# Kernel tuning notes

Hardware: AMD Instinct MI355X
Metric: run time of the kernel (lower is better)

Reference implementation:

```python
import jax, jax.numpy as jnp
import numpy as np

SIGMA = 1.0


def setup_inputs() -> dict:
    key = jax.random.key(0)
    k1, k2 = jax.random.split(key)
    B, N = 32, 1024
    logits = jax.random.normal(k1, (B, N, 1), dtype=jnp.float32)
    labels = jax.random.randint(k2, (B, N, 1), 0, 5).astype(jnp.float32)
    item_mask = jnp.ones((B, N), dtype=bool)
    return {"logits": logits, "labels": labels, "item_mask": item_mask}


def _ndcg_weights(y, sorted_indices):
    # y: (B, N) relevance labels; sorted_indices: (B, N) argsort of scores desc
    b, n = y.shape
    gains = 2.0 ** y - 1.0                                   # (B, N)
    ideal_sorted = -jnp.sort(-gains, axis=-1)                # descending sort
    positions = jnp.arange(1, n + 1, dtype=y.dtype)          # (N,)
    discounts = 1.0 / jnp.log2(positions + 1.0)              # (N,)  (k=None)
    idcg = jnp.clip((ideal_sorted * discounts).sum(-1, keepdims=True), 1e-8)
    # scatter: ranks[b, sorted_indices[b, j]] = j + 1
    ranks = jnp.zeros_like(y).at[jnp.arange(b)[:, None], sorted_indices].set(
        jnp.broadcast_to(positions, (b, n)))
    disc_i = 1.0 / jnp.log2(ranks + 1.0)                     # (B, N)
    gain_diff = jnp.abs(gains[:, :, None] - gains[:, None, :])   # (B, N, N)
    disc_diff = jnp.abs(disc_i[:, :, None] - disc_i[:, None, :]) # (B, N, N)
    return gain_diff * disc_diff / idcg[..., None]


def reference(logits, labels, item_mask):
    scores = logits[..., 0]                                  # (B, N)
    y = labels[..., 0].astype(jnp.float32)                   # (B, N)
    n = scores.shape[1]
    sorted_indices = jnp.argsort(-jax.lax.stop_gradient(scores), axis=-1)
    s_ij = SIGMA * (scores[:, :, None] - scores[:, None, :])     # (B, N, N)
    y_ij = jnp.sign(y[:, :, None] - y[:, None, :])               # (B, N, N)
    weights = _ndcg_weights(y, sorted_indices)                   # (B, N, N)
    pair_loss = jax.nn.softplus(-y_ij * s_ij) * weights          # log1p(exp(.))
    triu = jnp.triu(jnp.ones((n, n), dtype=bool), k=1)
    valid = item_mask[:, :, None] & item_mask[:, None, :]
    pair_loss = pair_loss * triu[None] * valid
    loss = pair_loss.sum(axis=(1, 2))                            # (B,)
    return loss.mean()                                           # reduction='mean'
```

## Files before the change

kernel.cpp:

```cpp
#include <hip/hip_runtime.h>
#include <math.h>


#define N    1024
#define T    1024
#define BPB  8

typedef unsigned int u32;

__device__ __forceinline__ float pair_term(const float4 fi, const float4 fj)
{
    const float ds  = fi.x - fj.x;
    const float dg  = fi.y - fj.y;
    const float arg = (dg > 0.0f) ? -ds : ds;
    const float sp  = __logf(1.0f + __expf(arg));
    return sp * fabsf(dg) * fabsf(fi.z - fj.z);
}

__device__ __forceinline__ u32 flipkey(float s)
{
    const u32 u = __float_as_uint(s);
    const u32 m = (u >> 31) ? ~u : (u | 0x80000000u);
    return ~m;
}

__global__ __launch_bounds__(T) void lrank_fused(const float* __restrict__ logits,
                                                 const float* __restrict__ labels,
                                                 float* __restrict__ out,
                                                 float inv_B)
{
    __shared__ float4 it[N];
    __shared__ u32    shi[N];
    __shared__ u32    slo[N];
    __shared__ float  wred[16];
    __shared__ float  wredI[16];
    __shared__ int    hist[5];
    __shared__ float  sidcg;

    const int b  = blockIdx.y;
    const int c  = blockIdx.x;
    const int t  = threadIdx.x;
    const int wv = t >> 6;
    const int ln = t & 63;

    if (t < 5) hist[t] = 0;
    __syncthreads();

    if (t < 256) {
        const float4 sv = ((const float4*)(logits + b * N))[t];
        const float4 yv = ((const float4*)(labels + b * N))[t];
        it[4*t+0] = make_float4(sv.x, exp2f(yv.x) - 1.0f, 0.0f, 0.0f);
        it[4*t+1] = make_float4(sv.y, exp2f(yv.y) - 1.0f, 0.0f, 0.0f);
        it[4*t+2] = make_float4(sv.z, exp2f(yv.z) - 1.0f, 0.0f, 0.0f);
        it[4*t+3] = make_float4(sv.w, exp2f(yv.w) - 1.0f, 0.0f, 0.0f);
        shi[4*t+0] = flipkey(sv.x);  slo[4*t+0] = 4*t+0;
        shi[4*t+1] = flipkey(sv.y);  slo[4*t+1] = 4*t+1;
        shi[4*t+2] = flipkey(sv.z);  slo[4*t+2] = 4*t+2;
        shi[4*t+3] = flipkey(sv.w);  slo[4*t+3] = 4*t+3;
    } else if (t < 512) {
        const int uu = t - 256;
        const float4 yv = ((const float4*)(labels + b * N))[uu];
        atomicAdd(&hist[(int)yv.x], 1);
        atomicAdd(&hist[(int)yv.y], 1);
        atomicAdd(&hist[(int)yv.z], 1);
        atomicAdd(&hist[(int)yv.w], 1);
    }
    __syncthreads();

    {
        const int c4 = hist[4];
        const int c3 = c4 + hist[3];
        const int c2 = c3 + hist[2];
        const int c1 = c2 + hist[1];
        const float gain = (t < c4) ? 15.0f : (t < c3) ? 7.0f
                         : (t < c2) ? 3.0f  : (t < c1) ? 1.0f : 0.0f;
        float ip = gain / __log2f((float)(t + 2));
        #pragma unroll
        for (int off = 32; off; off >>= 1) ip += __shfl_xor(ip, off);
        if (ln == 0) wredI[wv] = ip;
    }

    for (int k = 2; k <= N; k <<= 1) {
        for (int jj = k >> 1; jj > 0; jj >>= 1) {
            if (t < 512) {
                const int i  = ((t & ~(jj - 1)) << 1) | (t & (jj - 1));
                const int ix = i | jj;
                const u32 ha = shi[i],  hb = shi[ix];
                const u32 la = slo[i],  lb = slo[ix];
                const bool up  = ((i & k) == 0);
                const bool agt = (ha > hb) || (ha == hb && la > lb);
                if (agt == up) {
                    shi[i] = hb; shi[ix] = ha;
                    slo[i] = lb; slo[ix] = la;
                }
            }
            __syncthreads();
        }
    }

    it[slo[t]].z = 1.0f / __log2f((float)(t + 2));
    __syncthreads();
    if (t == 0) {
        float s = 0.0f;
        #pragma unroll
        for (int i2 = 0; i2 < 16; ++i2) s += wredI[i2];
        sidcg = fmaxf(s, 1e-8f);
    }
    __syncthreads();

    const int rA = c * 64 + 4 * wv;
    const int rB = 1023 - rA;
    const float4 fr0 = it[rA],     fr1 = it[rA + 1];
    const float4 fr2 = it[rA + 2], fr3 = it[rA + 3];
    const float4 gr0 = it[rB],     gr1 = it[rB - 1];
    const float4 gr2 = it[rB - 2], gr3 = it[rB - 3];

    float acc = 0.0f;
    for (int j = rA + 1 + ln; j < N; j += 64) {
        const float4 fj = it[j];
        acc += pair_term(fr0, fj);
        if (j > rA + 1) acc += pair_term(fr1, fj);
        if (j > rA + 2) acc += pair_term(fr2, fj);
        if (j > rA + 3) acc += pair_term(fr3, fj);
    }
    for (int j = rB - 2 + ln; j < N; j += 64) {
        const float4 fj = it[j];
        acc += pair_term(gr3, fj);
        if (j > rB - 2) acc += pair_term(gr2, fj);
        if (j > rB - 1) acc += pair_term(gr1, fj);
        if (j > rB)     acc += pair_term(gr0, fj);
    }

    #pragma unroll
    for (int off = 32; off; off >>= 1) acc += __shfl_xor(acc, off);
    if (ln == 0) wred[wv] = acc;
    __syncthreads();
    if (t == 0) {
        float s = 0.0f;
        #pragma unroll
        for (int i2 = 0; i2 < 16; ++i2) s += wred[i2];
        atomicAdd(out, s * inv_B / sidcg);
    }
}

extern "C" void kernel_launch(void* const* d_in, const int* in_sizes, int n_in,
                              void* d_out, int out_size, void* d_ws, size_t ws_size,
                              hipStream_t stream) {
    const float* logits = (const float*)d_in[0];
    const float* labels = (const float*)d_in[1];
    const int B = in_sizes[0] / N;
    float* out = (float*)d_out;

    hipMemsetAsync(out, 0, sizeof(float), stream);
    lrank_fused<<<dim3(BPB, B), dim3(T), 0, stream>>>(logits, labels, out,
                                                      1.0f / (float)B);
}
```

Baseline: 85.40 us.

## Register-resident bitonic sort with wave shuffles, ballot histogram, base-2 softplus

Replaces the shared-memory bitonic sort, which had a barrier per step and only 512 active threads, with a per-thread 64-bit key sort. Stages with stride under 64 use wave shuffles and larger strides exchange through LDS, which cuts the number of block-wide barriers. The label histogram now uses ballot/popcount instead of per-element LDS atomics. Scores are prescaled by log2(e) so softplus can use exp2/log2, with ln2 folded into the final scale. The triangular diagonal pairs are peeled into a small prologue so the main pair loops run without branches. In exchange, the kernel adds shuffle traffic and more complex index logic.

After: 79.88 us. -6.5%, faster.

```diff
diff --git a/kernel.cpp b/kernel.cpp
--- a/kernel.cpp
+++ b/kernel.cpp
@@ -7,15 +7,7 @@
 #define BPB  8
 
 typedef unsigned int u32;
-
-__device__ __forceinline__ float pair_term(const float4 fi, const float4 fj)
-{
-    const float ds  = fi.x - fj.x;
-    const float dg  = fi.y - fj.y;
-    const float arg = (dg > 0.0f) ? -ds : ds;
-    const float sp  = __logf(1.0f + __expf(arg));
-    return sp * fabsf(dg) * fabsf(fi.z - fj.z);
-}
+typedef unsigned long long u64;
 
 __device__ __forceinline__ u32 flipkey(float s)
 {
@@ -24,14 +16,29 @@
     return ~m;
 }
 
+__device__ __forceinline__ u64 shfl_xor_u64(u64 v, int m)
+{
+    const int lo = __shfl_xor((int)(u32)v, m);
+    const int hi = __shfl_xor((int)(u32)(v >> 32), m);
+    return ((u64)(u32)hi << 32) | (u32)lo;
+}
+
+__device__ __forceinline__ float pair_term(const float4 fi, const float4 fj)
+{
+    const float d1  = fj.x - fi.x;
+    const float dg  = fi.y - fj.y;
+    const float arg = (dg > 0.0f) ? d1 : -d1;
+    const float sp2 = log2f(1.0f + exp2f(arg));
+    return sp2 * fabsf(dg) * fabsf(fi.z - fj.z);
+}
+
 __global__ __launch_bounds__(T) void lrank_fused(const float* __restrict__ logits,
                                                  const float* __restrict__ labels,
                                                  float* __restrict__ out,
-                                                 float inv_B)
+                                                 float scale)
 {
     __shared__ float4 it[N];
-    __shared__ u32    shi[N];
-    __shared__ u32    slo[N];
+    __shared__ u64    sk[N];
     __shared__ float  wred[16];
     __shared__ float  wredI[16];
     __shared__ int    hist[5];
@@ -46,24 +53,16 @@
     if (t < 5) hist[t] = 0;
     __syncthreads();
 
-    if (t < 256) {
-        const float4 sv = ((const float4*)(logits + b * N))[t];
-        const float4 yv = ((const float4*)(labels + b * N))[t];
-        it[4*t+0] = make_float4(sv.x, exp2f(yv.x) - 1.0f, 0.0f, 0.0f);
-        it[4*t+1] = make_float4(sv.y, exp2f(yv.y) - 1.0f, 0.0f, 0.0f);
-        it[4*t+2] = make_float4(sv.z, exp2f(yv.z) - 1.0f, 0.0f, 0.0f);
-        it[4*t+3] = make_float4(sv.w, exp2f(yv.w) - 1.0f, 0.0f, 0.0f);
-        shi[4*t+0] = flipkey(sv.x);  slo[4*t+0] = 4*t+0;
-        shi[4*t+1] = flipkey(sv.y);  slo[4*t+1] = 4*t+1;
-        shi[4*t+2] = flipkey(sv.z);  slo[4*t+2] = 4*t+2;
-        shi[4*t+3] = flipkey(sv.w);  slo[4*t+3] = 4*t+3;
-    } else if (t < 512) {
-        const int uu = t - 256;
-        const float4 yv = ((const float4*)(labels + b * N))[uu];
-        atomicAdd(&hist[(int)yv.x], 1);
-        atomicAdd(&hist[(int)yv.y], 1);
-        atomicAdd(&hist[(int)yv.z], 1);
-        atomicAdd(&hist[(int)yv.w], 1);
+    const float s = logits[b * N + t];
+    const float y = labels[b * N + t];
+    it[t] = make_float4(s * 1.4426950408889634f, exp2f(y) - 1.0f, 0.0f, 0.0f);
+    u64 K = ((u64)flipkey(s) << 32) | (u32)t;
+
+    const int yi = (int)y;
+    #pragma unroll
+    for (int v = 0; v < 5; ++v) {
+        const u64 m = __ballot(yi == v);
+        if (ln == 0) atomicAdd(&hist[v], (int)__popcll(m));
     }
     __syncthreads();
 
@@ -80,31 +79,43 @@
         if (ln == 0) wredI[wv] = ip;
     }
 
-    for (int k = 2; k <= N; k <<= 1) {
-        for (int jj = k >> 1; jj > 0; jj >>= 1) {
-            if (t < 512) {
-                const int i  = ((t & ~(jj - 1)) << 1) | (t & (jj - 1));
-                const int ix = i | jj;
-                const u32 ha = shi[i],  hb = shi[ix];
-                const u32 la = slo[i],  lb = slo[ix];
-                const bool up  = ((i & k) == 0);
-                const bool agt = (ha > hb) || (ha == hb && la > lb);
-                if (agt == up) {
-                    shi[i] = hb; shi[ix] = ha;
-                    slo[i] = lb; slo[ix] = la;
-                }
-            }
+    #pragma unroll
+    for (int k = 2; k <= 64; k <<= 1) {
+        #pragma unroll
+        for (int jj = k >> 1; jj; jj >>= 1) {
+            const u64 PK = shfl_xor_u64(K, jj);
+            const bool keepmin = (((t & k) == 0) == ((t & jj) == 0));
+            const bool mine_gt = (K > PK);
+            if (mine_gt == keepmin) K = PK;
+        }
+    }
+    #pragma unroll
+    for (int k = 128; k <= 1024; k <<= 1) {
+        #pragma unroll
+        for (int jj = k >> 1; jj >= 64; jj >>= 1) {
+            sk[t] = K;
             __syncthreads();
+            const u64 PK = sk[t ^ jj];
+            const bool keepmin = (((t & k) == 0) == ((t & jj) == 0));
+            const bool mine_gt = (K > PK);
+            if (mine_gt == keepmin) K = PK;
+            __syncthreads();
+        }
+        #pragma unroll
+        for (int jj = 32; jj; jj >>= 1) {
+            const u64 PK = shfl_xor_u64(K, jj);
+            const bool keepmin = (((t & k) == 0) == ((t & jj) == 0));
+            const bool mine_gt = (K > PK);
+            if (mine_gt == keepmin) K = PK;
         }
     }
 
-    it[slo[t]].z = 1.0f / __log2f((float)(t + 2));
-    __syncthreads();
+    it[(int)(K & 1023u)].z = 1.0f / __log2f((float)(t + 2));
     if (t == 0) {
-        float s = 0.0f;
+        float si = 0.0f;
         #pragma unroll
-        for (int i2 = 0; i2 < 16; ++i2) s += wredI[i2];
-        sidcg = fmaxf(s, 1e-8f);
+        for (int i = 0; i < 16; ++i) si += wredI[i];
+        sidcg = fmaxf(si, 1e-8f);
     }
     __syncthreads();
 
@@ -116,19 +127,30 @@
     const float4 gr2 = it[rB - 2], gr3 = it[rB - 3];
 
     float acc = 0.0f;
-    for (int j = rA + 1 + ln; j < N; j += 64) {
+
+    if (ln < 12) {
+        const int p = (ln >= 6) ? ln - 6 : ln;
+        const int a = (p < 3) ? 0 : (p < 5) ? 1 : 2;
+        const int bb = (p == 0) ? 1 : (p == 1) ? 2 : (p == 2) ? 3
+                     : (p == 3) ? 2 : 3;
+        const int i1 = (ln < 6) ? rA + a  : rB - a;
+        const int i2 = (ln < 6) ? rA + bb : rB - bb;
+        acc += pair_term(it[i1], it[i2]);
+    }
+
+    for (int j = rA + 4 + ln; j < N; j += 64) {
         const float4 fj = it[j];
         acc += pair_term(fr0, fj);
-        if (j > rA + 1) acc += pair_term(fr1, fj);
-        if (j > rA + 2) acc += pair_term(fr2, fj);
-        if (j > rA + 3) acc += pair_term(fr3, fj);
+        acc += pair_term(fr1, fj);
+        acc += pair_term(fr2, fj);
+        acc += pair_term(fr3, fj);
     }
-    for (int j = rB - 2 + ln; j < N; j += 64) {
+    for (int j = rB + 1 + ln; j < N; j += 64) {
         const float4 fj = it[j];
+        acc += pair_term(gr0, fj);
+        acc += pair_term(gr1, fj);
+        acc += pair_term(gr2, fj);
         acc += pair_term(gr3, fj);
-        if (j > rB - 2) acc += pair_term(gr2, fj);
-        if (j > rB - 1) acc += pair_term(gr1, fj);
-        if (j > rB)     acc += pair_term(gr0, fj);
     }
 
     #pragma unroll
@@ -136,10 +158,10 @@
     if (ln == 0) wred[wv] = acc;
     __syncthreads();
     if (t == 0) {
-        float s = 0.0f;
+        float sm = 0.0f;
         #pragma unroll
-        for (int i2 = 0; i2 < 16; ++i2) s += wred[i2];
-        atomicAdd(out, s * inv_B / sidcg);
+        for (int i = 0; i < 16; ++i) sm += wred[i];
+        atomicAdd(out, sm * scale / sidcg);
     }
 }
 
@@ -153,5 +175,5 @@
 
     hipMemsetAsync(out, 0, sizeof(float), stream);
     lrank_fused<<<dim3(BPB, B), dim3(T), 0, stream>>>(logits, labels, out,
-                                                      1.0f / (float)B);
+                                                      0.6931471805599453f / (float)B);
 }
```
